# Kernel optimization log

Measured on AMD Instinct MI355X. Metric: run time of the kernel, lower is better.

The kernel has to match this reference:

```python
import jax, jax.numpy as jnp
import numpy as np

NUM_CLASSES = 10
GAMMA = 1.0
EPS = 1e-12


def setup_inputs() -> dict:
    key = jax.random.key(0)
    k1, k2, k3, k4 = jax.random.split(key, 4)
    x = jax.random.normal(k1, (1024, 64), dtype=jnp.float32)
    exemplars = jax.random.normal(k2, (50000, 64), dtype=jnp.float32)
    exemplar_labels = jax.random.randint(k3, (50000,), 0, NUM_CLASSES)
    # beta_raw initialized as softplus^{-1}(init_beta) with init_beta=1.0
    init_beta = 1.0
    beta_raw = jnp.array([np.log(np.exp(init_beta) - 1.0)], dtype=jnp.float32)
    return {"x": x, "exemplars": exemplars, "exemplar_labels": exemplar_labels,
            "beta_raw": beta_raw}


def reference(x, exemplars, exemplar_labels, beta_raw):
    # Squared Euclidean distances (weight_diag == ones) via GEMM expansion:
    # d2[b, e] = ||x_b||^2 + ||e_e||^2 - 2 <x_b, e_e>
    x2 = jnp.sum(x * x, axis=-1, keepdims=True)            # (B, 1)
    e2 = jnp.sum(exemplars * exemplars, axis=-1)           # (Ne,)
    d2 = x2 + e2[None, :] - 2.0 * (x @ exemplars.T)        # (B, Ne)
    d2 = jnp.maximum(d2, 0.0)  # true sq-dist is nonneg; guards GEMM round-off
    beta = jax.nn.softplus(beta_raw[0])
    sims = jnp.exp(-beta * d2)                              # (B, Ne)
    # scatter-add similarities into per-class bins: (C, B) -> (B, C)
    class_sims = jax.ops.segment_sum(sims.T, exemplar_labels,
                                     num_segments=NUM_CLASSES).T
    logits = GAMMA * jnp.log(class_sims + EPS)
    return logits
```

## Files before the change

kernel.cpp:

```cpp
#include <hip/hip_runtime.h>


#define NB      1024
#define NE      50000
#define NCHUNK  98
#define KD      64
#define NC      10
#define SROWS   64
#define NSTAGE  8
#define LROW    72
#define BCOLS   128

#define LOG2E   1.4426950408889634f

using half8   = __attribute__((ext_vector_type(8))) _Float16;
using half4v  = __attribute__((ext_vector_type(4))) _Float16;
using floatx4 = __attribute__((ext_vector_type(4))) float;

__device__ __forceinline__ float softplus_f(float x) {
  return (x > 20.f) ? x : log1pf(__expf(x));
}

__device__ __forceinline__ float exp2_hw(float x) {
#if __has_builtin(__builtin_amdgcn_exp2f)
  return __builtin_amdgcn_exp2f(x);
#else
  return exp2f(x);
#endif
}

__global__ __launch_bounds__(256) void main_kernel(
    const float* __restrict__ x, const float* __restrict__ ex,
    const int* __restrict__ labels, const float* __restrict__ beta_raw,
    float* __restrict__ part)
{
  __shared__ _Float16 Ah[2][SROWS * LROW];
  __shared__ float    Ce[2][SROWS];
  __shared__ int      Lb[2][SROWS];

  const int tid  = threadIdx.x;
  const int wave = tid >> 6;
  const int lane = tid & 63;
  const int l15  = lane & 15;
  const int quad = lane >> 4;

  const int btile = blockIdx.x;
  const int chunk = blockIdx.y;
  const int e0    = chunk * 512;
  const int bm0   = btile * BCOLS + wave * 16;
  const int bm1   = bm0 + 64;

  const float beta = softplus_f(beta_raw[0]);
  const float nb2  = -beta * LOG2E;
  const float s2   = 2.f * beta * LOG2E;

  const float* xr0 = x + (size_t)(bm0 + l15) * KD;
  const float* xr1 = x + (size_t)(bm1 + l15) * KD;
  const float4 xa0 = *(const float4*)(xr0 + quad * 8);
  const float4 xa1 = *(const float4*)(xr0 + quad * 8 + 4);
  const float4 xa2 = *(const float4*)(xr0 + quad * 8 + 32);
  const float4 xa3 = *(const float4*)(xr0 + quad * 8 + 36);
  const float4 xb0 = *(const float4*)(xr1 + quad * 8);
  const float4 xb1 = *(const float4*)(xr1 + quad * 8 + 4);
  const float4 xb2 = *(const float4*)(xr1 + quad * 8 + 32);
  const float4 xb3 = *(const float4*)(xr1 + quad * 8 + 36);

  const half8 bx00 = { (_Float16)xa0.x, (_Float16)xa0.y, (_Float16)xa0.z, (_Float16)xa0.w,
                       (_Float16)xa1.x, (_Float16)xa1.y, (_Float16)xa1.z, (_Float16)xa1.w };
  const half8 bx01 = { (_Float16)xa2.x, (_Float16)xa2.y, (_Float16)xa2.z, (_Float16)xa2.w,
                       (_Float16)xa3.x, (_Float16)xa3.y, (_Float16)xa3.z, (_Float16)xa3.w };
  const half8 bx10 = { (_Float16)xb0.x, (_Float16)xb0.y, (_Float16)xb0.z, (_Float16)xb0.w,
                       (_Float16)xb1.x, (_Float16)xb1.y, (_Float16)xb1.z, (_Float16)xb1.w };
  const half8 bx11 = { (_Float16)xb2.x, (_Float16)xb2.y, (_Float16)xb2.z, (_Float16)xb2.w,
                       (_Float16)xb3.x, (_Float16)xb3.y, (_Float16)xb3.z, (_Float16)xb3.w };

  float sx0 = xa0.x*xa0.x + xa0.y*xa0.y + xa0.z*xa0.z + xa0.w*xa0.w
            + xa1.x*xa1.x + xa1.y*xa1.y + xa1.z*xa1.z + xa1.w*xa1.w
            + xa2.x*xa2.x + xa2.y*xa2.y + xa2.z*xa2.z + xa2.w*xa2.w
            + xa3.x*xa3.x + xa3.y*xa3.y + xa3.z*xa3.z + xa3.w*xa3.w;
  float sx1 = xb0.x*xb0.x + xb0.y*xb0.y + xb0.z*xb0.z + xb0.w*xb0.w
            + xb1.x*xb1.x + xb1.y*xb1.y + xb1.z*xb1.z + xb1.w*xb1.w
            + xb2.x*xb2.x + xb2.y*xb2.y + xb2.z*xb2.z + xb2.w*xb2.w
            + xb3.x*xb3.x + xb3.y*xb3.y + xb3.z*xb3.z + xb3.w*xb3.w;
  sx0 += __shfl_xor(sx0, 16, 64);  sx0 += __shfl_xor(sx0, 32, 64);
  sx1 += __shfl_xor(sx1, 16, 64);  sx1 += __shfl_xor(sx1, 32, 64);
  const float cb0l = nb2 * sx0;
  const float cb1l = nb2 * sx1;

  const int srow = tid >> 2;
  const int scol = tid & 3;
  const int lofs = srow * LROW + scol * 16;

  float4 pf0, pf1, pf2, pf3;
  int    prl;
  bool   pvalid;

  auto stage_load = [&](int st) {
    const int grow = e0 + st * SROWS + srow;
    pvalid = grow < NE;
    pf0 = make_float4(0.f, 0.f, 0.f, 0.f);
    pf1 = pf0; pf2 = pf0; pf3 = pf0;
    prl = 0;
    if (pvalid) {
      const float* g = ex + (size_t)grow * KD + scol * 16;
      pf0 = *(const float4*)(g);
      pf1 = *(const float4*)(g + 4);
      pf2 = *(const float4*)(g + 8);
      pf3 = *(const float4*)(g + 12);
      if (scol == 1) prl = labels[grow];
    }
  };

  auto stage_write = [&](int buf) {
    float sn = pf0.x*pf0.x + pf0.y*pf0.y + pf0.z*pf0.z + pf0.w*pf0.w
             + pf1.x*pf1.x + pf1.y*pf1.y + pf1.z*pf1.z + pf1.w*pf1.w
             + pf2.x*pf2.x + pf2.y*pf2.y + pf2.z*pf2.z + pf2.w*pf2.w
             + pf3.x*pf3.x + pf3.y*pf3.y + pf3.z*pf3.z + pf3.w*pf3.w;
    sn += __shfl_xor(sn, 1, 64);
    sn += __shfl_xor(sn, 2, 64);
    const half8 h0 = { (_Float16)pf0.x, (_Float16)pf0.y, (_Float16)pf0.z, (_Float16)pf0.w,
                       (_Float16)pf1.x, (_Float16)pf1.y, (_Float16)pf1.z, (_Float16)pf1.w };
    const half8 h1 = { (_Float16)pf2.x, (_Float16)pf2.y, (_Float16)pf2.z, (_Float16)pf2.w,
                       (_Float16)pf3.x, (_Float16)pf3.y, (_Float16)pf3.z, (_Float16)pf3.w };
    *(half8*)(&Ah[buf][lofs])     = h0;
    *(half8*)(&Ah[buf][lofs + 8]) = h1;
    if (scol == 0) Ce[buf][srow] = pvalid ? (nb2 * sn) : -1e30f;
    if (scol == 1) Lb[buf][srow] = prl;
  };

  stage_load(0);
  stage_write(0);
  __syncthreads();

  floatx4 acc0 = {0.f, 0.f, 0.f, 0.f};
  floatx4 acc1 = {0.f, 0.f, 0.f, 0.f};

  for (int st = 0; st < NSTAGE; ++st) {
    const int b = st & 1;

    if (st + 1 < NSTAGE) stage_load(st + 1);

    #pragma unroll
    for (int sub = 0; sub < 4; ++sub) {
      const int abase = (sub * 16 + l15) * LROW + quad * 8;
      const half8 ae0 = *(const half8*)(&Ah[b][abase]);
      const half8 ae1 = *(const half8*)(&Ah[b][abase + 32]);
      const float4 ce4 = *(const float4*)(&Ce[b][sub * 16 + quad * 4]);
      const int4   lb4 = *(const int4*)(&Lb[b][sub * 16 + quad * 4]);

      floatx4 d0 = {0.f, 0.f, 0.f, 0.f};
      floatx4 d1 = {0.f, 0.f, 0.f, 0.f};
      d0 = __builtin_amdgcn_mfma_f32_16x16x32_f16(ae0, bx00, d0, 0, 0, 0);
      d0 = __builtin_amdgcn_mfma_f32_16x16x32_f16(ae1, bx01, d0, 0, 0, 0);
      d1 = __builtin_amdgcn_mfma_f32_16x16x32_f16(ae0, bx10, d1, 0, 0, 0);
      d1 = __builtin_amdgcn_mfma_f32_16x16x32_f16(ae1, bx11, d1, 0, 0, 0);

      const float cef[4] = { ce4.x, ce4.y, ce4.z, ce4.w };
      float t0[4], t1[4];
      #pragma unroll
      for (int r = 0; r < 4; ++r) {
        t0[r] = fminf(fmaf(s2, d0[r], cb0l + cef[r]), 0.f);
        t1[r] = fminf(fmaf(s2, d1[r], cb1l + cef[r]), 0.f);
      }

      const float m0 = fmaxf(fmaxf(t0[0], t0[1]), fmaxf(t0[2], t0[3]));
      const float m1 = fmaxf(fmaxf(t1[0], t1[1]), fmaxf(t1[2], t1[3]));
      if (__any(fmaxf(m0, m1) > -25.f)) {
        half4v oh;
        oh[0] = (lb4.x == l15) ? (_Float16)1.f : (_Float16)0.f;
        oh[1] = (lb4.y == l15) ? (_Float16)1.f : (_Float16)0.f;
        oh[2] = (lb4.z == l15) ? (_Float16)1.f : (_Float16)0.f;
        oh[3] = (lb4.w == l15) ? (_Float16)1.f : (_Float16)0.f;

        half4v p0, p1;
        #pragma unroll
        for (int r = 0; r < 4; ++r) {
          p0[r] = (_Float16)exp2_hw(t0[r]);
          p1[r] = (_Float16)exp2_hw(t1[r]);
        }

        acc0 = __builtin_amdgcn_mfma_f32_16x16x16f16(oh, p0, acc0, 0, 0, 0);
        acc1 = __builtin_amdgcn_mfma_f32_16x16x16f16(oh, p1, acc1, 0, 0, 0);
      }
    }

    if (st + 1 < NSTAGE) {
      stage_write((st + 1) & 1);
      __syncthreads();
    }
  }

  float* dst = part + (size_t)chunk * (NB * NC);
  #pragma unroll
  for (int r = 0; r < 4; ++r) {
    const int c = quad * 4 + r;
    if (c < NC) {
      dst[(bm0 + l15) * NC + c] = acc0[r];
      dst[(bm1 + l15) * NC + c] = acc1[r];
    }
  }
}

__global__ __launch_bounds__(256) void reduce_kernel(
    const float* __restrict__ part, float* __restrict__ out)
{
  const int bc = blockIdx.x * 256 + threadIdx.x;
  if (bc < NB * NC) {
    float s = 0.f;
    #pragma unroll 7
    for (int k = 0; k < NCHUNK; ++k) s += part[(size_t)k * (NB * NC) + bc];
    out[bc] = __logf(s + 1e-12f);
  }
}

extern "C" void kernel_launch(void* const* d_in, const int* in_sizes, int n_in,
                              void* d_out, int out_size, void* d_ws, size_t ws_size,
                              hipStream_t stream)
{
  const float* x        = (const float*)d_in[0];
  const float* ex       = (const float*)d_in[1];
  const int*   labels   = (const int*)d_in[2];
  const float* beta_raw = (const float*)d_in[3];
  float* out = (float*)d_out;

  float* part = (float*)d_ws;

  dim3 g(NB / BCOLS, NCHUNK);
  main_kernel<<<g, 256, 0, stream>>>(x, ex, labels, beta_raw, part);
  reduce_kernel<<<40, 256, 0, stream>>>(part, out);
}
```

Baseline: 94.47 us.

## Widen batch tile to 256 columns and preload chunk labels into shared memory

```diff
diff --git a/kernel.cpp b/kernel.cpp
--- a/kernel.cpp
+++ b/kernel.cpp
@@ -8,8 +8,10 @@
 #define NC      10
 #define SROWS   64
 #define NSTAGE  8
+#define CROWS   512
 #define LROW    72
-#define BCOLS   128
+#define BCOLS   256
+#define NGRP    4
 
 #define LOG2E   1.4426950408889634f
 
@@ -36,7 +38,7 @@
 {
   __shared__ _Float16 Ah[2][SROWS * LROW];
   __shared__ float    Ce[2][SROWS];
-  __shared__ int      Lb[2][SROWS];
+  __shared__ int      Lb_all[CROWS];
 
   const int tid  = threadIdx.x;
   const int wave = tid >> 6;
@@ -46,53 +48,47 @@
 
   const int btile = blockIdx.x;
   const int chunk = blockIdx.y;
-  const int e0    = chunk * 512;
+  const int e0    = chunk * CROWS;
   const int bm0   = btile * BCOLS + wave * 16;
-  const int bm1   = bm0 + 64;
 
   const float beta = softplus_f(beta_raw[0]);
   const float nb2  = -beta * LOG2E;
   const float s2   = 2.f * beta * LOG2E;
 
-  const float* xr0 = x + (size_t)(bm0 + l15) * KD;
-  const float* xr1 = x + (size_t)(bm1 + l15) * KD;
-  const float4 xa0 = *(const float4*)(xr0 + quad * 8);
-  const float4 xa1 = *(const float4*)(xr0 + quad * 8 + 4);
-  const float4 xa2 = *(const float4*)(xr0 + quad * 8 + 32);
-  const float4 xa3 = *(const float4*)(xr0 + quad * 8 + 36);
-  const float4 xb0 = *(const float4*)(xr1 + quad * 8);
-  const float4 xb1 = *(const float4*)(xr1 + quad * 8 + 4);
-  const float4 xb2 = *(const float4*)(xr1 + quad * 8 + 32);
-  const float4 xb3 = *(const float4*)(xr1 + quad * 8 + 36);
-
-  const half8 bx00 = { (_Float16)xa0.x, (_Float16)xa0.y, (_Float16)xa0.z, (_Float16)xa0.w,
-                       (_Float16)xa1.x, (_Float16)xa1.y, (_Float16)xa1.z, (_Float16)xa1.w };
-  const half8 bx01 = { (_Float16)xa2.x, (_Float16)xa2.y, (_Float16)xa2.z, (_Float16)xa2.w,
-                       (_Float16)xa3.x, (_Float16)xa3.y, (_Float16)xa3.z, (_Float16)xa3.w };
-  const half8 bx10 = { (_Float16)xb0.x, (_Float16)xb0.y, (_Float16)xb0.z, (_Float16)xb0.w,
-                       (_Float16)xb1.x, (_Float16)xb1.y, (_Float16)xb1.z, (_Float16)xb1.w };
-  const half8 bx11 = { (_Float16)xb2.x, (_Float16)xb2.y, (_Float16)xb2.z, (_Float16)xb2.w,
-                       (_Float16)xb3.x, (_Float16)xb3.y, (_Float16)xb3.z, (_Float16)xb3.w };
-
-  float sx0 = xa0.x*xa0.x + xa0.y*xa0.y + xa0.z*xa0.z + xa0.w*xa0.w
-            + xa1.x*xa1.x + xa1.y*xa1.y + xa1.z*xa1.z + xa1.w*xa1.w
-            + xa2.x*xa2.x + xa2.y*xa2.y + xa2.z*xa2.z + xa2.w*xa2.w
-            + xa3.x*xa3.x + xa3.y*xa3.y + xa3.z*xa3.z + xa3.w*xa3.w;
-  float sx1 = xb0.x*xb0.x + xb0.y*xb0.y + xb0.z*xb0.z + xb0.w*xb0.w
-            + xb1.x*xb1.x + xb1.y*xb1.y + xb1.z*xb1.z + xb1.w*xb1.w
-            + xb2.x*xb2.x + xb2.y*xb2.y + xb2.z*xb2.z + xb2.w*xb2.w
-            + xb3.x*xb3.x + xb3.y*xb3.y + xb3.z*xb3.z + xb3.w*xb3.w;
-  sx0 += __shfl_xor(sx0, 16, 64);  sx0 += __shfl_xor(sx0, 32, 64);
-  sx1 += __shfl_xor(sx1, 16, 64);  sx1 += __shfl_xor(sx1, 32, 64);
-  const float cb0l = nb2 * sx0;
-  const float cb1l = nb2 * sx1;
+  #pragma unroll
+  for (int i = 0; i < CROWS / 256; ++i) {
+    const int r = i * 256 + tid;
+    const int grow = e0 + r;
+    Lb_all[r] = (grow < NE) ? labels[grow] : 0;
+  }
+
+  half8 bx[NGRP][2];
+  float cbl[NGRP];
+  #pragma unroll
+  for (int g = 0; g < NGRP; ++g) {
+    const float* xr = x + (size_t)(bm0 + 64 * g + l15) * KD;
+    const float4 v0 = *(const float4*)(xr + quad * 8);
+    const float4 v1 = *(const float4*)(xr + quad * 8 + 4);
+    const float4 v2 = *(const float4*)(xr + quad * 8 + 32);
+    const float4 v3 = *(const float4*)(xr + quad * 8 + 36);
+    bx[g][0] = half8{ (_Float16)v0.x, (_Float16)v0.y, (_Float16)v0.z, (_Float16)v0.w,
+                      (_Float16)v1.x, (_Float16)v1.y, (_Float16)v1.z, (_Float16)v1.w };
+    bx[g][1] = half8{ (_Float16)v2.x, (_Float16)v2.y, (_Float16)v2.z, (_Float16)v2.w,
+                      (_Float16)v3.x, (_Float16)v3.y, (_Float16)v3.z, (_Float16)v3.w };
+    float s = v0.x*v0.x + v0.y*v0.y + v0.z*v0.z + v0.w*v0.w
+            + v1.x*v1.x + v1.y*v1.y + v1.z*v1.z + v1.w*v1.w
+            + v2.x*v2.x + v2.y*v2.y + v2.z*v2.z + v2.w*v2.w
+            + v3.x*v3.x + v3.y*v3.y + v3.z*v3.z + v3.w*v3.w;
+    s += __shfl_xor(s, 16, 64);
+    s += __shfl_xor(s, 32, 64);
+    cbl[g] = nb2 * s;
+  }
 
   const int srow = tid >> 2;
   const int scol = tid & 3;
   const int lofs = srow * LROW + scol * 16;
 
   float4 pf0, pf1, pf2, pf3;
-  int    prl;
   bool   pvalid;
 
   auto stage_load = [&](int st) {
@@ -100,14 +96,12 @@
     pvalid = grow < NE;
     pf0 = make_float4(0.f, 0.f, 0.f, 0.f);
     pf1 = pf0; pf2 = pf0; pf3 = pf0;
-    prl = 0;
     if (pvalid) {
       const float* g = ex + (size_t)grow * KD + scol * 16;
       pf0 = *(const float4*)(g);
       pf1 = *(const float4*)(g + 4);
       pf2 = *(const float4*)(g + 8);
       pf3 = *(const float4*)(g + 12);
-      if (scol == 1) prl = labels[grow];
     }
   };
 
@@ -125,15 +119,15 @@
     *(half8*)(&Ah[buf][lofs])     = h0;
     *(half8*)(&Ah[buf][lofs + 8]) = h1;
     if (scol == 0) Ce[buf][srow] = pvalid ? (nb2 * sn) : -1e30f;
-    if (scol == 1) Lb[buf][srow] = prl;
   };
 
   stage_load(0);
   stage_write(0);
   __syncthreads();
 
-  floatx4 acc0 = {0.f, 0.f, 0.f, 0.f};
-  floatx4 acc1 = {0.f, 0.f, 0.f, 0.f};
+  floatx4 acc[NGRP];
+  #pragma unroll
+  for (int g = 0; g < NGRP; ++g) acc[g] = floatx4{0.f, 0.f, 0.f, 0.f};
 
   for (int st = 0; st < NSTAGE; ++st) {
     const int b = st & 1;
@@ -146,41 +140,43 @@
       const half8 ae0 = *(const half8*)(&Ah[b][abase]);
       const half8 ae1 = *(const half8*)(&Ah[b][abase + 32]);
       const float4 ce4 = *(const float4*)(&Ce[b][sub * 16 + quad * 4]);
-      const int4   lb4 = *(const int4*)(&Lb[b][sub * 16 + quad * 4]);
-
-      floatx4 d0 = {0.f, 0.f, 0.f, 0.f};
-      floatx4 d1 = {0.f, 0.f, 0.f, 0.f};
-      d0 = __builtin_amdgcn_mfma_f32_16x16x32_f16(ae0, bx00, d0, 0, 0, 0);
-      d0 = __builtin_amdgcn_mfma_f32_16x16x32_f16(ae1, bx01, d0, 0, 0, 0);
-      d1 = __builtin_amdgcn_mfma_f32_16x16x32_f16(ae0, bx10, d1, 0, 0, 0);
-      d1 = __builtin_amdgcn_mfma_f32_16x16x32_f16(ae1, bx11, d1, 0, 0, 0);
+      const int4   lb4 = *(const int4*)(&Lb_all[st * SROWS + sub * 16 + quad * 4]);
+
+      floatx4 d[NGRP];
+      #pragma unroll
+      for (int g = 0; g < NGRP; ++g) {
+        floatx4 t = {0.f, 0.f, 0.f, 0.f};
+        t = __builtin_amdgcn_mfma_f32_16x16x32_f16(ae0, bx[g][0], t, 0, 0, 0);
+        t = __builtin_amdgcn_mfma_f32_16x16x32_f16(ae1, bx[g][1], t, 0, 0, 0);
+        d[g] = t;
+      }
 
       const float cef[4] = { ce4.x, ce4.y, ce4.z, ce4.w };
-      float t0[4], t1[4];
-      #pragma unroll
-      for (int r = 0; r < 4; ++r) {
-        t0[r] = fminf(fmaf(s2, d0[r], cb0l + cef[r]), 0.f);
-        t1[r] = fminf(fmaf(s2, d1[r], cb1l + cef[r]), 0.f);
-      }
-
-      const float m0 = fmaxf(fmaxf(t0[0], t0[1]), fmaxf(t0[2], t0[3]));
-      const float m1 = fmaxf(fmaxf(t1[0], t1[1]), fmaxf(t1[2], t1[3]));
-      if (__any(fmaxf(m0, m1) > -25.f)) {
+      float t[NGRP][4];
+      #pragma unroll
+      for (int g = 0; g < NGRP; ++g)
+        #pragma unroll
+        for (int r = 0; r < 4; ++r)
+          t[g][r] = fminf(fmaf(s2, d[g][r], cbl[g] + cef[r]), 0.f);
+
+      float m = -1e30f;
+      #pragma unroll
+      for (int g = 0; g < NGRP; ++g)
+        m = fmaxf(m, fmaxf(fmaxf(t[g][0], t[g][1]), fmaxf(t[g][2], t[g][3])));
+      if (__any(m > -25.f)) {
         half4v oh;
         oh[0] = (lb4.x == l15) ? (_Float16)1.f : (_Float16)0.f;
         oh[1] = (lb4.y == l15) ? (_Float16)1.f : (_Float16)0.f;
         oh[2] = (lb4.z == l15) ? (_Float16)1.f : (_Float16)0.f;
         oh[3] = (lb4.w == l15) ? (_Float16)1.f : (_Float16)0.f;
 
-        half4v p0, p1;
         #pragma unroll
-        for (int r = 0; r < 4; ++r) {
-          p0[r] = (_Float16)exp2_hw(t0[r]);
-          p1[r] = (_Float16)exp2_hw(t1[r]);
+        for (int g = 0; g < NGRP; ++g) {
+          half4v p;
+          #pragma unroll
+          for (int r = 0; r < 4; ++r) p[r] = (_Float16)exp2_hw(t[g][r]);
+          acc[g] = __builtin_amdgcn_mfma_f32_16x16x16f16(oh, p, acc[g], 0, 0, 0);
         }
-
-        acc0 = __builtin_amdgcn_mfma_f32_16x16x16f16(oh, p0, acc0, 0, 0, 0);
-        acc1 = __builtin_amdgcn_mfma_f32_16x16x16f16(oh, p1, acc1, 0, 0, 0);
       }
     }
 
@@ -195,8 +191,9 @@
   for (int r = 0; r < 4; ++r) {
     const int c = quad * 4 + r;
     if (c < NC) {
-      dst[(bm0 + l15) * NC + c] = acc0[r];
-      dst[(bm1 + l15) * NC + c] = acc1[r];
+      #pragma unroll
+      for (int g = 0; g < NGRP; ++g)
+        dst[(bm0 + 64 * g + l15) * NC + c] = acc[g][r];
     }
   }
 }
```

Result: no change. 94.65 us (+0.2%).

## Preload chunk labels into LDS and skip storing all-zero partial blocks

Applied to the files above, without the earlier changes.

```diff
diff --git a/kernel.cpp b/kernel.cpp
--- a/kernel.cpp
+++ b/kernel.cpp
@@ -8,8 +8,10 @@
 #define NC      10
 #define SROWS   64
 #define NSTAGE  8
+#define CROWS   512
 #define LROW    72
 #define BCOLS   128
+#define NBT     (NB / BCOLS)
 
 #define LOG2E   1.4426950408889634f
 
@@ -32,11 +34,12 @@
 __global__ __launch_bounds__(256) void main_kernel(
     const float* __restrict__ x, const float* __restrict__ ex,
     const int* __restrict__ labels, const float* __restrict__ beta_raw,
-    float* __restrict__ part)
+    float* __restrict__ part, int* __restrict__ flags)
 {
   __shared__ _Float16 Ah[2][SROWS * LROW];
   __shared__ float    Ce[2][SROWS];
-  __shared__ int      Lb[2][SROWS];
+  __shared__ int      Lb_all[CROWS];
+  __shared__ int      blockLive;
 
   const int tid  = threadIdx.x;
   const int wave = tid >> 6;
@@ -46,13 +49,21 @@
 
   const int btile = blockIdx.x;
   const int chunk = blockIdx.y;
-  const int e0    = chunk * 512;
+  const int e0    = chunk * CROWS;
   const int bm0   = btile * BCOLS + wave * 16;
   const int bm1   = bm0 + 64;
 
   const float beta = softplus_f(beta_raw[0]);
   const float nb2  = -beta * LOG2E;
   const float s2   = 2.f * beta * LOG2E;
+
+  #pragma unroll
+  for (int i = 0; i < CROWS / 256; ++i) {
+    const int r = i * 256 + tid;
+    const int grow = e0 + r;
+    Lb_all[r] = (grow < NE) ? labels[grow] : 0;
+  }
+  if (tid == 0) blockLive = 0;
 
   const float* xr0 = x + (size_t)(bm0 + l15) * KD;
   const float* xr1 = x + (size_t)(bm1 + l15) * KD;
@@ -92,7 +103,6 @@
   const int lofs = srow * LROW + scol * 16;
 
   float4 pf0, pf1, pf2, pf3;
-  int    prl;
   bool   pvalid;
 
   auto stage_load = [&](int st) {
@@ -100,14 +110,12 @@
     pvalid = grow < NE;
     pf0 = make_float4(0.f, 0.f, 0.f, 0.f);
     pf1 = pf0; pf2 = pf0; pf3 = pf0;
-    prl = 0;
     if (pvalid) {
       const float* g = ex + (size_t)grow * KD + scol * 16;
       pf0 = *(const float4*)(g);
       pf1 = *(const float4*)(g + 4);
       pf2 = *(const float4*)(g + 8);
       pf3 = *(const float4*)(g + 12);
-      if (scol == 1) prl = labels[grow];
     }
   };
 
@@ -125,7 +133,6 @@
     *(half8*)(&Ah[buf][lofs])     = h0;
     *(half8*)(&Ah[buf][lofs + 8]) = h1;
     if (scol == 0) Ce[buf][srow] = pvalid ? (nb2 * sn) : -1e30f;
-    if (scol == 1) Lb[buf][srow] = prl;
   };
 
   stage_load(0);
@@ -146,7 +153,7 @@
       const half8 ae0 = *(const half8*)(&Ah[b][abase]);
       const half8 ae1 = *(const half8*)(&Ah[b][abase + 32]);
       const float4 ce4 = *(const float4*)(&Ce[b][sub * 16 + quad * 4]);
-      const int4   lb4 = *(const int4*)(&Lb[b][sub * 16 + quad * 4]);
+      const int4   lb4 = *(const int4*)(&Lb_all[st * SROWS + sub * 16 + quad * 4]);
 
       floatx4 d0 = {0.f, 0.f, 0.f, 0.f};
       floatx4 d1 = {0.f, 0.f, 0.f, 0.f};
@@ -190,25 +197,39 @@
     }
   }
 
-  float* dst = part + (size_t)chunk * (NB * NC);
+  bool ll = false;
   #pragma unroll
-  for (int r = 0; r < 4; ++r) {
-    const int c = quad * 4 + r;
-    if (c < NC) {
-      dst[(bm0 + l15) * NC + c] = acc0[r];
-      dst[(bm1 + l15) * NC + c] = acc1[r];
-    }
-  }
+  for (int r = 0; r < 4; ++r) ll |= (acc0[r] != 0.f) | (acc1[r] != 0.f);
+  __syncthreads();
+  if (__any(ll) && lane == 0) blockLive = 1;
+  __syncthreads();
+
+  if (blockLive) {
+    float* dst = part + (size_t)chunk * (NB * NC);
+    #pragma unroll
+    for (int r = 0; r < 4; ++r) {
+      const int c = quad * 4 + r;
+      if (c < NC) {
+        dst[(bm0 + l15) * NC + c] = acc0[r];
+        dst[(bm1 + l15) * NC + c] = acc1[r];
+      }
+    }
+  }
+  if (tid == 0) flags[btile * NCHUNK + chunk] = blockLive;
 }
 
 __global__ __launch_bounds__(256) void reduce_kernel(
-    const float* __restrict__ part, float* __restrict__ out)
+    const float* __restrict__ part, const int* __restrict__ flags,
+    float* __restrict__ out)
 {
   const int bc = blockIdx.x * 256 + threadIdx.x;
   if (bc < NB * NC) {
+    const int rbtile = bc / (BCOLS * NC);
+    const int fbase  = rbtile * NCHUNK;
     float s = 0.f;
-    #pragma unroll 7
-    for (int k = 0; k < NCHUNK; ++k) s += part[(size_t)k * (NB * NC) + bc];
+    for (int k = 0; k < NCHUNK; ++k) {
+      if (flags[fbase + k]) s += part[(size_t)k * (NB * NC) + bc];
+    }
     out[bc] = __logf(s + 1e-12f);
   }
 }
@@ -223,9 +244,11 @@
   const float* beta_raw = (const float*)d_in[3];
   float* out = (float*)d_out;
 
-  float* part = (float*)d_ws;
-
-  dim3 g(NB / BCOLS, NCHUNK);
-  main_kernel<<<g, 256, 0, stream>>>(x, ex, labels, beta_raw, part);
-  reduce_kernel<<<40, 256, 0, stream>>>(part, out);
-}
+  char* ws = (char*)d_ws;
+  float* part  = (float*)ws;
+  int*   flags = (int*)(ws + (size_t)NCHUNK * NB * NC * 4);
+
+  dim3 g(NBT, NCHUNK);
+  main_kernel<<<g, 256, 0, stream>>>(x, ex, labels, beta_raw, part, flags);
+  reduce_kernel<<<40, 256, 0, stream>>>(part, flags, out);
+}
```

Measured after the change: 97.93 us. 3.7% more time.
